# Performance work log

Measured on AMD Instinct MI355X. Metric: run time of the kernel, lower is better.

## Reference

```python
import jax, jax.numpy as jnp
import numpy as np

MARGIN = 0.02
EPS = 1e-12


def setup_inputs() -> dict:
    key = jax.random.key(0)
    n, d, k = 4096, 128, 4  # n anchors, embed dim, instances per class
    inputs = jax.random.normal(key, (n, d), dtype=jnp.float32)
    # Balanced, class-grouped batch (required by the original resize trick):
    # label of sample i is i // k.
    targets = (jnp.arange(n) // k).astype(jnp.int32)
    return {"inputs": inputs, "targets": targets, "num_instances": k}


def reference(inputs, targets, num_instances):
    n = inputs.shape[0]
    k = num_instances  # static python int

    # Pairwise euclidean distances (same math as euclidean_dist)
    sq = jnp.sum(inputs * inputs, axis=1, keepdims=True)  # [n,1]
    dist = sq + sq.T - 2.0 * (inputs @ inputs.T)          # [n,n]
    dist = jnp.sqrt(jnp.clip(dist, EPS, None))

    # Structured pos/neg indices for a grouped balanced batch
    # (equivalent to masked_select + resize in the original).
    row = jnp.arange(n)
    class_start = (row // k) * k        # first index of anchor's class block
    pos_in_class = row % k              # anchor's slot within its class
    o_pos = jnp.arange(k - 1)
    # same-class indices excluding self -> [n, k-1]
    pos_idx = class_start[:, None] + o_pos[None, :] + (o_pos[None, :] >= pos_in_class[:, None])
    o_neg = jnp.arange(n - k)
    # all indices outside the anchor's class block -> [n, n-k]
    neg_idx = o_neg[None, :] + k * (o_neg[None, :] >= class_start[:, None])

    pos_dist = dist[row[:, None], pos_idx]  # [n, k-1]
    neg_dist = dist[row[:, None], neg_idx]  # [n, n-k]

    # Triplet margin matrix per anchor: trip[i, m, j] = d_pos[i,j] - d_neg[i,m] + margin
    trip = pos_dist[:, None, :] - neg_dist[:, :, None] + MARGIN  # [n, n-k, k-1]
    mask = trip > 0
    num_valid = jnp.sum(mask)
    total = jnp.sum(jnp.where(mask, trip, 0.0))
    denom = jnp.maximum(num_valid, 1).astype(trip.dtype)
    loss = jnp.where(num_valid > 0, total / denom, jnp.zeros((), trip.dtype))

    per_anchor_valid = jnp.sum(mask, axis=(1, 2))  # [n]
    accuracy = jnp.mean((per_anchor_valid == 0).astype(jnp.float32))
    pos_d = jnp.mean(pos_dist)
    neg_d = jnp.mean(neg_dist)
    return loss, accuracy, pos_d, neg_d
```

## Files before the change

kernel.cpp:

```cpp
#include <hip/hip_runtime.h>

#define NROWS 4096
#define DIM   128
#define KCLS  4
#define NBLK  1056
#define MARGIN_F 0.02f
#define EPS_F    1e-12f

typedef unsigned short ushort_t;
typedef unsigned int   uint_t;
typedef __attribute__((ext_vector_type(8)))  short bf16x8;
typedef __attribute__((ext_vector_type(16))) float f32x16;

__device__ __forceinline__ ushort_t rne_bf16(float v, float& back) {
    uint_t u = __float_as_uint(v);
    uint_t r = (u + 0x7fffu + ((u >> 16) & 1u)) >> 16;
    back = __uint_as_float(r << 16);
    return (ushort_t)r;
}

__device__ __forceinline__ bf16x8 pack8(const ushort_t* h) {
    bf16x8 v;
#pragma unroll
    for (int e = 0; e < 8; ++e) v[e] = (short)h[e];
    return v;
}

__device__ __forceinline__ float fsqrt(float x) {
    float r;
    asm("v_sqrt_f32 %0, %1" : "=v"(r) : "v"(x));
    return r;
}

__device__ __forceinline__ void blk_decode(int bid, int& ti, int& tJ) {
    tJ = (int)((sqrtf((float)(4 * bid + 1)) - 1.0f) * 0.5f);
    while ((tJ + 1) * (tJ + 2) <= bid) ++tJ;
    while (tJ * (tJ + 1) > bid) --tJ;
    ti = bid - tJ * (tJ + 1);
}

__global__ __launch_bounds__(256) void k_prep(
    const float* __restrict__ x,
    float4* __restrict__ spd,
    ushort_t* __restrict__ xf,
    uint_t* __restrict__ imask, uint_t* __restrict__ jmask)
{
    if (blockIdx.x == 0) {
        const int tt = threadIdx.x;
        if (tt < 128) imask[tt] = 0u; else jmask[tt - 128] = 0u;
    }
    const int wave = threadIdx.x >> 6, lane = threadIdx.x & 63;
    const int cls  = (blockIdx.x << 2) + wave;
    const int r0   = lane >> 4;
    const int cseg = lane & 15;
    const int row  = (cls << 2) + r0;

    const float4* rp = (const float4*)(x + (size_t)row * DIM + (cseg << 3));
    const float4 v0 = rp[0], v1 = rp[1];
    float vs[8] = {v0.x, v0.y, v0.z, v0.w, v1.x, v1.y, v1.z, v1.w};

    float sq = 0.f;
#pragma unroll
    for (int e = 0; e < 8; ++e) sq = fmaf(vs[e], vs[e], sq);
#pragma unroll
    for (int off = 1; off < 16; off <<= 1) sq += __shfl_xor(sq, off, 16);

    float sq4[4];
#pragma unroll
    for (int s = 0; s < 4; ++s) sq4[s] = __shfl(sq, (s << 4) | cseg);

    float dl[3];
#pragma unroll
    for (int delta = 1; delta <= 3; ++delta) {
        const int p = r0 ^ delta;
        float dot = 0.f;
#pragma unroll
        for (int e = 0; e < 8; ++e) {
            const float o = __shfl(vs[e], (p << 4) | cseg);
            dot = fmaf(vs[e], o, dot);
        }
#pragma unroll
        for (int off = 1; off < 16; off <<= 1) dot += __shfl_xor(dot, off, 16);
        dl[delta - 1] = fsqrt(fmaxf(sq4[r0] + sq4[p] - 2.f * dot, EPS_F));
    }
    float po[3];
#pragma unroll
    for (int o = 0; o < 3; ++o) {
        const int s = o + (o >= r0 ? 1 : 0);
        const int d = r0 ^ s;
        po[o] = (d == 1) ? dl[0] : (d == 2) ? dl[1] : dl[2];
    }
    if (cseg == 0) spd[row] = make_float4(sq4[r0], po[0], po[1], po[2]);

    ushort_t hs[8], ls[8];
#pragma unroll
    for (int e = 0; e < 8; ++e) {
        float back, d_;
        hs[e] = rne_bf16(vs[e], back);
        ls[e] = rne_bf16(vs[e] - back, d_);
    }
    const int band = row >> 5, L = row & 31, cb = cseg >> 1, sf = cseg & 1;
    ushort_t* dst = xf + ((size_t)((band << 3) + cb) << 1) * 512
                       + (((sf << 5) + L) << 3);
    *(bf16x8*)dst         = pack8(hs);
    *(bf16x8*)(dst + 512) = pack8(ls);
}

__global__ __launch_bounds__(256, 4) void k_tiles(
    const ushort_t* __restrict__ xf,
    const float4* __restrict__ spd,
    uint_t* __restrict__ imask, uint_t* __restrict__ jmask,
    float4* __restrict__ partial)
{
    int ti, tJ;
    blk_decode((int)blockIdx.x, ti, tJ);

    const int t = threadIdx.x, wave = t >> 6, lane = t & 63;
    const int wr = wave >> 1, wc = wave & 1;
    const int col = lane & 31, hi = lane >> 5;
    const int ibase = ti << 6;
    const int tj64 = (tJ << 1) + wc;
    const bool active   = (tj64 >= ti);
    const bool anchor_j = (tj64 > ti);
    const int jb  = (tJ << 2) + (wc << 1);
    const int jg0 = (jb << 5) + col;
    const int jg1 = jg0 + 32;

    __shared__ float4 spd_i[64];
    __shared__ float4 wpart[4];

    float4 myspd;
    if (t < 64) myspd = spd[ibase + t];
    const float4 sj0 = spd[jg0];
    const float4 sj1 = spd[jg1];

    const ushort_t* pa  = xf + (size_t)((ti << 1) + wr) * 8192 + lane * 8;
    const ushort_t* pb0 = xf + (size_t)jb * 8192 + lane * 8;
    const ushort_t* pb1 = pb0 + 8192;

    f32x16 acc0, acc1;
#pragma unroll
    for (int r = 0; r < 16; ++r) { acc0[r] = 0.f; acc1[r] = 0.f; }

#pragma unroll
    for (int c = 0; c < 8; ++c) {
        const bf16x8 ah  = *(const bf16x8*)(pa  + c * 1024);
        const bf16x8 al  = *(const bf16x8*)(pa  + c * 1024 + 512);
        const bf16x8 b0h = *(const bf16x8*)(pb0 + c * 1024);
        const bf16x8 b0l = *(const bf16x8*)(pb0 + c * 1024 + 512);
        const bf16x8 b1h = *(const bf16x8*)(pb1 + c * 1024);
        const bf16x8 b1l = *(const bf16x8*)(pb1 + c * 1024 + 512);
        acc0 = __builtin_amdgcn_mfma_f32_32x32x16_bf16(ah, b0h, acc0, 0, 0, 0);
        acc1 = __builtin_amdgcn_mfma_f32_32x32x16_bf16(ah, b1h, acc1, 0, 0, 0);
        acc0 = __builtin_amdgcn_mfma_f32_32x32x16_bf16(ah, b0l, acc0, 0, 0, 0);
        acc1 = __builtin_amdgcn_mfma_f32_32x32x16_bf16(ah, b1l, acc1, 0, 0, 0);
        acc0 = __builtin_amdgcn_mfma_f32_32x32x16_bf16(al, b0h, acc0, 0, 0, 0);
        acc1 = __builtin_amdgcn_mfma_f32_32x32x16_bf16(al, b1h, acc1, 0, 0, 0);
    }

    if (t < 64) spd_i[t] = myspd;
    __syncthreads();

    float ts = 0.f, ns = 0.f, cntf = 0.f;
    uint_t iam = 0, jany0 = 0, jany1 = 0;

    if (active) {
        const int jcls0 = jg0 >> 2, jcls1 = jg1 >> 2;
        const float nsw = anchor_j ? 2.f : 1.f;
#pragma unroll
        for (int r = 0; r < 16; ++r) {
            const int src = (r & 3) + ((r >> 2) << 3) + (hi << 2);
            const float4 si = spd_i[(wr << 5) + src];
            const int icls = (ibase + (wr << 5) + src) >> 2;

            {
                const float dd = fsqrt(fmaxf(si.x + sj0.x - 2.f * acc0[r], EPS_F));
                const bool skip = !anchor_j && (icls == jcls0);
                if (!skip) {
                    ns += nsw * dd;
                    uint_t v = 0; float h;
                    h = si.y + MARGIN_F - dd; if (h > 0.f) { ts += h; cntf += 1.f; v = 1u; }
                    h = si.z + MARGIN_F - dd; if (h > 0.f) { ts += h; cntf += 1.f; v = 1u; }
                    h = si.w + MARGIN_F - dd; if (h > 0.f) { ts += h; cntf += 1.f; v = 1u; }
                    iam |= v << r;
                    if (anchor_j) {
                        h = sj0.y + MARGIN_F - dd; if (h > 0.f) { ts += h; cntf += 1.f; jany0 = 1u; }
                        h = sj0.z + MARGIN_F - dd; if (h > 0.f) { ts += h; cntf += 1.f; jany0 = 1u; }
                        h = sj0.w + MARGIN_F - dd; if (h > 0.f) { ts += h; cntf += 1.f; jany0 = 1u; }
                    }
                }
            }
            {
                const float dd = fsqrt(fmaxf(si.x + sj1.x - 2.f * acc1[r], EPS_F));
                const bool skip = !anchor_j && (icls == jcls1);
                if (!skip) {
                    ns += nsw * dd;
                    uint_t v = 0; float h;
                    h = si.y + MARGIN_F - dd; if (h > 0.f) { ts += h; cntf += 1.f; v = 1u; }
                    h = si.z + MARGIN_F - dd; if (h > 0.f) { ts += h; cntf += 1.f; v = 1u; }
                    h = si.w + MARGIN_F - dd; if (h > 0.f) { ts += h; cntf += 1.f; v = 1u; }
                    iam |= v << r;
                    if (anchor_j) {
                        h = sj1.y + MARGIN_F - dd; if (h > 0.f) { ts += h; cntf += 1.f; jany1 = 1u; }
                        h = sj1.z + MARGIN_F - dd; if (h > 0.f) { ts += h; cntf += 1.f; jany1 = 1u; }
                        h = sj1.w + MARGIN_F - dd; if (h > 0.f) { ts += h; cntf += 1.f; jany1 = 1u; }
                    }
                }
            }
        }

        uint_t iam_all = iam;
#pragma unroll
        for (int off = 1; off < 32; off <<= 1)
            iam_all |= __shfl_xor(iam_all, off);
        uint_t rowmask = 0;
#pragma unroll
        for (int r = 0; r < 16; ++r)
            if ((iam_all >> r) & 1u)
                rowmask |= 1u << ((r & 3) + ((r >> 2) << 3) + (hi << 2));
        if ((lane == 0 || lane == 32) && rowmask)
            atomicOr(&imask[(ti << 1) + wr], rowmask);

        if (anchor_j) {
            const unsigned long long b0 = __ballot(jany0 != 0);
            const uint_t m0 = (uint_t)b0 | (uint_t)(b0 >> 32);
            if (lane == 0 && m0) atomicOr(&jmask[jb], m0);
            const unsigned long long b1 = __ballot(jany1 != 0);
            const uint_t m1 = (uint_t)b1 | (uint_t)(b1 >> 32);
            if (lane == 0 && m1) atomicOr(&jmask[jb + 1], m1);
        }
    }

#pragma unroll
    for (int off = 32; off; off >>= 1) {
        ts   += __shfl_down(ts, off);
        ns   += __shfl_down(ns, off);
        cntf += __shfl_down(cntf, off);
    }
    if (lane == 0) wpart[wave] = make_float4(ts, ns, cntf, 0.f);
    __syncthreads();
    if (t == 0) {
        float4 s = wpart[0];
        s.x += wpart[1].x + wpart[2].x + wpart[3].x;
        s.y += wpart[1].y + wpart[2].y + wpart[3].y;
        s.z += wpart[1].z + wpart[2].z + wpart[3].z;
        partial[blockIdx.x] = s;
    }
}

__global__ void k_final(const uint_t* __restrict__ imask,
                        const uint_t* __restrict__ jmask,
                        const float4* __restrict__ partial,
                        const float4* __restrict__ spd,
                        float* __restrict__ out)
{
    const int t = threadIdx.x;
    const int lane = t & 63, wave = t >> 6;
    double ts = 0.0, ns = 0.0, cnt = 0.0, ps = 0.0;
    uint_t zc = 0;

    for (int idx = t; idx < NBLK; idx += 1024) {
        const float4 p = partial[idx];
        ts += (double)p.x; ns += (double)p.y; cnt += (double)p.z;
    }
    for (int idx = t; idx < NROWS; idx += 1024) {
        const float4 p = spd[idx];
        ps += (double)p.y + (double)p.z + (double)p.w;
    }
    if (t < 128) zc = 32u - (uint_t)__popc(imask[t] | jmask[t]);

#pragma unroll
    for (int off = 32; off; off >>= 1) {
        ts  += __shfl_down(ts, off);
        ns  += __shfl_down(ns, off);
        cnt += __shfl_down(cnt, off);
        ps  += __shfl_down(ps, off);
        zc  += __shfl_down(zc, off);
    }
    __shared__ double s0[16], s1[16], s2[16], s3[16];
    __shared__ uint_t s4[16];
    if (lane == 0) { s0[wave]=ts; s1[wave]=ns; s2[wave]=cnt; s3[wave]=ps; s4[wave]=zc; }
    __syncthreads();
    if (t == 0) {
        double a0=0, a1=0, a2=0, a3=0; uint_t a4=0;
#pragma unroll
        for (int w = 0; w < 16; ++w) { a0+=s0[w]; a1+=s1[w]; a2+=s2[w]; a3+=s3[w]; a4+=s4[w]; }
        out[0] = (float)(a2 > 0.0 ? a0 / a2 : 0.0);
        out[1] = (float)((double)a4 / (double)NROWS);
        out[2] = (float)(a3 / ((double)NROWS * 3.0));
        out[3] = (float)(a1 / ((double)NROWS * (double)(NROWS - KCLS)));
    }
}

extern "C" void kernel_launch(void* const* d_in, const int* in_sizes, int n_in,
                              void* d_out, int out_size, void* d_ws, size_t ws_size,
                              hipStream_t stream)
{
    const float* x = (const float*)d_in[0];
    float* out = (float*)d_out;
    char* ws = (char*)d_ws;

    uint_t*   imask   = (uint_t*)(ws + 0);
    uint_t*   jmask   = (uint_t*)(ws + 512);
    float4*   spd     = (float4*)(ws + 1024);
    float4*   partial = (float4*)(ws + 1024 + 65536);
    ushort_t* xf      = (ushort_t*)(ws + 1024 + 65536 + 16896);

    k_prep<<<256, 256, 0, stream>>>(x, spd, xf, imask, jmask);
    k_tiles<<<NBLK, 256, 0, stream>>>(xf, spd, imask, jmask, partial);
    k_final<<<1, 1024, 0, stream>>>(imask, jmask, partial, spd, out);
}
```

Before: 111.0 us.

## Fuse final reduction into tile kernel via last-block counter and double-buffer loads

Removes the separate single-block final kernel by having the last tile block, detected through an atomic counter, run the global reduction. Positive-distance sums are pre-reduced per block in the prep kernel so the final step reads 256 floats instead of all of spd. The MFMA loop now prefetches the next K chunk into a second register set while the current one is multiplied. This saves one kernel launch and hides load latency, at the cost of more registers and a threadfence and atomic in every block.

```diff
diff --git a/kernel.cpp b/kernel.cpp
--- a/kernel.cpp
+++ b/kernel.cpp
@@ -39,15 +39,20 @@
     ti = bid - tJ * (tJ + 1);
 }
 
+#define LD(dst, base, off) dst = *(const bf16x8*)((base) + (off))
+
 __global__ __launch_bounds__(256) void k_prep(
     const float* __restrict__ x,
     float4* __restrict__ spd,
     ushort_t* __restrict__ xf,
-    uint_t* __restrict__ imask, uint_t* __restrict__ jmask)
+    uint_t* __restrict__ imask, uint_t* __restrict__ jmask,
+    uint_t* __restrict__ counter,
+    float* __restrict__ posp)
 {
     if (blockIdx.x == 0) {
         const int tt = threadIdx.x;
         if (tt < 128) imask[tt] = 0u; else jmask[tt - 128] = 0u;
+        if (tt == 0) *counter = 0u;
     }
     const int wave = threadIdx.x >> 6, lane = threadIdx.x & 63;
     const int cls  = (blockIdx.x << 2) + wave;
@@ -92,6 +97,15 @@
     }
     if (cseg == 0) spd[row] = make_float4(sq4[r0], po[0], po[1], po[2]);
 
+    float ppart = (cseg == 0) ? (po[0] + po[1] + po[2]) : 0.f;
+#pragma unroll
+    for (int off = 32; off; off >>= 1) ppart += __shfl_down(ppart, off);
+    __shared__ float pblk[4];
+    if (lane == 0) pblk[wave] = ppart;
+    __syncthreads();
+    if (threadIdx.x == 0)
+        posp[blockIdx.x] = pblk[0] + pblk[1] + pblk[2] + pblk[3];
+
     ushort_t hs[8], ls[8];
 #pragma unroll
     for (int e = 0; e < 8; ++e) {
@@ -110,7 +124,10 @@
     const ushort_t* __restrict__ xf,
     const float4* __restrict__ spd,
     uint_t* __restrict__ imask, uint_t* __restrict__ jmask,
-    float4* __restrict__ partial)
+    float4* __restrict__ partial,
+    uint_t* __restrict__ counter,
+    const float* __restrict__ posp,
+    float* __restrict__ out)
 {
     int ti, tJ;
     blk_decode((int)blockIdx.x, ti, tJ);
@@ -128,6 +145,7 @@
 
     __shared__ float4 spd_i[64];
     __shared__ float4 wpart[4];
+    __shared__ uint_t lastflag;
 
     float4 myspd;
     if (t < 64) myspd = spd[ibase + t];
@@ -142,20 +160,33 @@
 #pragma unroll
     for (int r = 0; r < 16; ++r) { acc0[r] = 0.f; acc1[r] = 0.f; }
 
-#pragma unroll
-    for (int c = 0; c < 8; ++c) {
-        const bf16x8 ah  = *(const bf16x8*)(pa  + c * 1024);
-        const bf16x8 al  = *(const bf16x8*)(pa  + c * 1024 + 512);
-        const bf16x8 b0h = *(const bf16x8*)(pb0 + c * 1024);
-        const bf16x8 b0l = *(const bf16x8*)(pb0 + c * 1024 + 512);
-        const bf16x8 b1h = *(const bf16x8*)(pb1 + c * 1024);
-        const bf16x8 b1l = *(const bf16x8*)(pb1 + c * 1024 + 512);
-        acc0 = __builtin_amdgcn_mfma_f32_32x32x16_bf16(ah, b0h, acc0, 0, 0, 0);
-        acc1 = __builtin_amdgcn_mfma_f32_32x32x16_bf16(ah, b1h, acc1, 0, 0, 0);
-        acc0 = __builtin_amdgcn_mfma_f32_32x32x16_bf16(ah, b0l, acc0, 0, 0, 0);
-        acc1 = __builtin_amdgcn_mfma_f32_32x32x16_bf16(ah, b1l, acc1, 0, 0, 0);
-        acc0 = __builtin_amdgcn_mfma_f32_32x32x16_bf16(al, b0h, acc0, 0, 0, 0);
-        acc1 = __builtin_amdgcn_mfma_f32_32x32x16_bf16(al, b1h, acc1, 0, 0, 0);
+    bf16x8 A0h, A0l, B0h, B0l, C0h, C0l;
+    bf16x8 A1h, A1l, B1h, B1l, C1h, C1l;
+    LD(A0h, pa, 0);   LD(A0l, pa, 512);
+    LD(B0h, pb0, 0);  LD(B0l, pb0, 512);
+    LD(C0h, pb1, 0);  LD(C0l, pb1, 512);
+#pragma unroll
+    for (int c = 0; c < 8; c += 2) {
+        LD(A1h, pa,  (c + 1) * 1024); LD(A1l, pa,  (c + 1) * 1024 + 512);
+        LD(B1h, pb0, (c + 1) * 1024); LD(B1l, pb0, (c + 1) * 1024 + 512);
+        LD(C1h, pb1, (c + 1) * 1024); LD(C1l, pb1, (c + 1) * 1024 + 512);
+        acc0 = __builtin_amdgcn_mfma_f32_32x32x16_bf16(A0h, B0h, acc0, 0, 0, 0);
+        acc1 = __builtin_amdgcn_mfma_f32_32x32x16_bf16(A0h, C0h, acc1, 0, 0, 0);
+        acc0 = __builtin_amdgcn_mfma_f32_32x32x16_bf16(A0h, B0l, acc0, 0, 0, 0);
+        acc1 = __builtin_amdgcn_mfma_f32_32x32x16_bf16(A0h, C0l, acc1, 0, 0, 0);
+        acc0 = __builtin_amdgcn_mfma_f32_32x32x16_bf16(A0l, B0h, acc0, 0, 0, 0);
+        acc1 = __builtin_amdgcn_mfma_f32_32x32x16_bf16(A0l, C0h, acc1, 0, 0, 0);
+        if (c + 2 < 8) {
+            LD(A0h, pa,  (c + 2) * 1024); LD(A0l, pa,  (c + 2) * 1024 + 512);
+            LD(B0h, pb0, (c + 2) * 1024); LD(B0l, pb0, (c + 2) * 1024 + 512);
+            LD(C0h, pb1, (c + 2) * 1024); LD(C0l, pb1, (c + 2) * 1024 + 512);
+        }
+        acc0 = __builtin_amdgcn_mfma_f32_32x32x16_bf16(A1h, B1h, acc0, 0, 0, 0);
+        acc1 = __builtin_amdgcn_mfma_f32_32x32x16_bf16(A1h, C1h, acc1, 0, 0, 0);
+        acc0 = __builtin_amdgcn_mfma_f32_32x32x16_bf16(A1h, B1l, acc0, 0, 0, 0);
+        acc1 = __builtin_amdgcn_mfma_f32_32x32x16_bf16(A1h, C1l, acc1, 0, 0, 0);
+        acc0 = __builtin_amdgcn_mfma_f32_32x32x16_bf16(A1l, B1h, acc0, 0, 0, 0);
+        acc1 = __builtin_amdgcn_mfma_f32_32x32x16_bf16(A1l, C1h, acc1, 0, 0, 0);
     }
 
     if (t < 64) spd_i[t] = myspd;
@@ -172,7 +203,6 @@
             const int src = (r & 3) + ((r >> 2) << 3) + (hi << 2);
             const float4 si = spd_i[(wr << 5) + src];
             const int icls = (ibase + (wr << 5) + src) >> 2;
-
             {
                 const float dd = fsqrt(fmaxf(si.x + sj0.x - 2.f * acc0[r], EPS_F));
                 const bool skip = !anchor_j && (icls == jcls0);
@@ -246,49 +276,44 @@
         s.z += wpart[1].z + wpart[2].z + wpart[3].z;
         partial[blockIdx.x] = s;
     }
-}
-
-__global__ void k_final(const uint_t* __restrict__ imask,
-                        const uint_t* __restrict__ jmask,
-                        const float4* __restrict__ partial,
-                        const float4* __restrict__ spd,
-                        float* __restrict__ out)
-{
-    const int t = threadIdx.x;
-    const int lane = t & 63, wave = t >> 6;
-    double ts = 0.0, ns = 0.0, cnt = 0.0, ps = 0.0;
-    uint_t zc = 0;
-
-    for (int idx = t; idx < NBLK; idx += 1024) {
-        const float4 p = partial[idx];
-        ts += (double)p.x; ns += (double)p.y; cnt += (double)p.z;
-    }
-    for (int idx = t; idx < NROWS; idx += 1024) {
-        const float4 p = spd[idx];
-        ps += (double)p.y + (double)p.z + (double)p.w;
-    }
-    if (t < 128) zc = 32u - (uint_t)__popc(imask[t] | jmask[t]);
-
-#pragma unroll
-    for (int off = 32; off; off >>= 1) {
-        ts  += __shfl_down(ts, off);
-        ns  += __shfl_down(ns, off);
-        cnt += __shfl_down(cnt, off);
-        ps  += __shfl_down(ps, off);
-        zc  += __shfl_down(zc, off);
-    }
-    __shared__ double s0[16], s1[16], s2[16], s3[16];
-    __shared__ uint_t s4[16];
-    if (lane == 0) { s0[wave]=ts; s1[wave]=ns; s2[wave]=cnt; s3[wave]=ps; s4[wave]=zc; }
+
+    __threadfence();
+    if (t == 0)
+        lastflag = (atomicAdd(counter, 1u) == NBLK - 1) ? 1u : 0u;
     __syncthreads();
-    if (t == 0) {
-        double a0=0, a1=0, a2=0, a3=0; uint_t a4=0;
-#pragma unroll
-        for (int w = 0; w < 16; ++w) { a0+=s0[w]; a1+=s1[w]; a2+=s2[w]; a3+=s3[w]; a4+=s4[w]; }
-        out[0] = (float)(a2 > 0.0 ? a0 / a2 : 0.0);
-        out[1] = (float)((double)a4 / (double)NROWS);
-        out[2] = (float)(a3 / ((double)NROWS * 3.0));
-        out[3] = (float)(a1 / ((double)NROWS * (double)(NROWS - KCLS)));
+    if (lastflag) {
+        __threadfence();
+
+        double fts = 0.0, fns = 0.0, fcnt = 0.0, fps = 0.0;
+        uint_t zc = 0;
+        for (int idx = t; idx < NBLK; idx += 256) {
+            const float4 p = partial[idx];
+            fts += (double)p.x; fns += (double)p.y; fcnt += (double)p.z;
+        }
+        if (t < 256) fps = (double)posp[t];
+        if (t < 128) zc = 32u - (uint_t)__popc(imask[t] | jmask[t]);
+
+#pragma unroll
+        for (int off = 32; off; off >>= 1) {
+            fts  += __shfl_down(fts, off);
+            fns  += __shfl_down(fns, off);
+            fcnt += __shfl_down(fcnt, off);
+            fps  += __shfl_down(fps, off);
+            zc   += __shfl_down(zc, off);
+        }
+        __shared__ double f0[4], f1[4], f2[4], f3[4];
+        __shared__ uint_t f4[4];
+        if (lane == 0) { f0[wave]=fts; f1[wave]=fns; f2[wave]=fcnt; f3[wave]=fps; f4[wave]=zc; }
+        __syncthreads();
+        if (t == 0) {
+            double a0=0, a1=0, a2=0, a3=0; uint_t a4=0;
+#pragma unroll
+            for (int w = 0; w < 4; ++w) { a0+=f0[w]; a1+=f1[w]; a2+=f2[w]; a3+=f3[w]; a4+=f4[w]; }
+            out[0] = (float)(a2 > 0.0 ? a0 / a2 : 0.0);
+            out[1] = (float)((double)a4 / (double)NROWS);
+            out[2] = (float)(a3 / ((double)NROWS * 3.0));
+            out[3] = (float)(a1 / ((double)NROWS * (double)(NROWS - KCLS)));
+        }
     }
 }
 
@@ -302,11 +327,13 @@
 
     uint_t*   imask   = (uint_t*)(ws + 0);
     uint_t*   jmask   = (uint_t*)(ws + 512);
-    float4*   spd     = (float4*)(ws + 1024);
-    float4*   partial = (float4*)(ws + 1024 + 65536);
-    ushort_t* xf      = (ushort_t*)(ws + 1024 + 65536 + 16896);
-
-    k_prep<<<256, 256, 0, stream>>>(x, spd, xf, imask, jmask);
-    k_tiles<<<NBLK, 256, 0, stream>>>(xf, spd, imask, jmask, partial);
-    k_final<<<1, 1024, 0, stream>>>(imask, jmask, partial, spd, out);
-}
+    uint_t*   counter = (uint_t*)(ws + 1024);
+    float*    posp    = (float*)(ws + 1088);
+    float4*   spd     = (float4*)(ws + 2112);
+    float4*   partial = (float4*)(ws + 2112 + 65536);
+    ushort_t* xf      = (ushort_t*)(ws + 2112 + 65536 + 16896);
+
+    k_prep<<<256, 256, 0, stream>>>(x, spd, xf, imask, jmask, counter, posp);
+    k_tiles<<<NBLK, 256, 0, stream>>>(xf, spd, imask, jmask, partial,
+                                      counter, posp, out);
+}
```

Result: slower. 164.2 us (+48.0%).
